# Performance work log

Hardware: AMD Instinct MI355X
Metric: run time of the kernel (lower is better)

The kernel has to match this reference:

```python
import jax, jax.numpy as jnp
import numpy as np


def setup_inputs() -> dict:
    key = jax.random.key(0)
    kq, kk, kv = jax.random.split(key, 3)
    B, T, H, D = 2, 4096, 8, 64
    q = jax.random.normal(kq, (B, T, H, D), dtype=jnp.float32)
    k = jax.random.normal(kk, (B, T, H, D), dtype=jnp.float32)
    v = jax.random.normal(kv, (B, T, H, D), dtype=jnp.float32)
    return {"q": q, "k": k, "v": v}


def reference(q, k, v):
    """Linear matrix-memory recurrence over the sequence:
       M_t = M_{t-1} + v_t k_t^T ;  y_t = M_t q_t
    q, k, v: [B, T, H, D] -> y: [B, T, H, D]
    """
    B, T, H, D = q.shape
    # time-major for scan: [T, B, H, D]
    qT = jnp.moveaxis(q, 1, 0)
    kT = jnp.moveaxis(k, 1, 0)
    vT = jnp.moveaxis(v, 1, 0)

    def step(M, qkv):
        q_t, k_t, v_t = qkv  # each [B, H, D]
        # update: M += v_t k_t^T  (outer product, 'bhd,bhe->bhde')
        M = M + v_t[..., :, None] * k_t[..., None, :]
        # apply: y_t = M q_t  ('bhde,bhe->bhd')
        y_t = jnp.einsum('bhde,bhe->bhd', M, q_t)
        return M, y_t

    M0 = jnp.zeros((B, H, D, D), dtype=q.dtype)
    _, ys = jax.lax.scan(step, M0, (qT, kT, vT))  # ys: [T, B, H, D]
    return jnp.moveaxis(ys, 0, 1)  # [B, T, H, D]
```

## Files before the change

kernel.cpp:

```cpp
#include <hip/hip_runtime.h>


#define B_   2
#define T_   4096
#define H_   8
#define D_   64
#define CH   64
#define NC   (T_ / CH)
#define BH   (B_ * H_)
#define SROW (H_ * D_)
#define SB   (T_ * H_ * D_)

typedef __attribute__((ext_vector_type(4))) float f32x4;
typedef __attribute__((ext_vector_type(8))) short bf16x8;

__device__ inline unsigned short f2bf(float f) {
  unsigned int u = __builtin_bit_cast(unsigned int, f);
  unsigned int r = (u + 0x7FFFu + ((u >> 16) & 1u)) >> 16;
  return (unsigned short)r;
}
__device__ inline float bf2f(unsigned short b) {
  unsigned int u = ((unsigned int)b) << 16;
  return __builtin_bit_cast(float, u);
}
__device__ inline void st4bf(unsigned short* p, float a, float b, float c, float d) {
  union { uint2 u; unsigned short s[4]; } x;
  x.s[0] = f2bf(a); x.s[1] = f2bf(b); x.s[2] = f2bf(c); x.s[3] = f2bf(d);
  *(uint2*)p = x.u;
}
__device__ inline bf16x8 ld128(const unsigned short* p) {
  union { uint4 u; bf16x8 v; } x;
  x.u = *(const uint4*)p;
  return x.v;
}
__device__ inline void unpackM(const uint4 a, const uint4 b, bf16x8& hi, bf16x8& lo) {
  unsigned xs[8] = { a.x, a.y, a.z, a.w, b.x, b.y, b.z, b.w };
  union { unsigned u[4]; bf16x8 v; } H, L;
#pragma unroll
  for (int i = 0; i < 4; ++i) {
    unsigned p0 = xs[2 * i], p1 = xs[2 * i + 1];
    H.u[i] = (p0 >> 16) | (p1 & 0xffff0000u);
    L.u[i] = (p0 & 0xffffu) | (p1 << 16);
  }
  hi = H.v; lo = L.v;
}


__global__ __launch_bounds__(256) void k_chunksum(const float* __restrict__ kp,
                                                  const float* __restrict__ vp,
                                                  unsigned short* __restrict__ Sp) {
  const int bid = blockIdx.x;
  const int c   = bid & 63;
  const int bh  = bid >> 6;
  const int b   = bh >> 3, h = bh & 7;
  const size_t base = (size_t)b * SB + (size_t)h * D_ + (size_t)(c * CH) * SROW;

  __shared__ __align__(16) unsigned short KT[4096], VT[4096];

  const int tid = threadIdx.x;
  const int l = tid & 63, w = tid >> 6;
  const int mlan = l & 15, qlan = l >> 4;

  {
    const int t0 = (tid >> 4) * 4;
    const int m0 = tid & 15;
    const int qs = (t0 >> 3) & 3, kbs = t0 >> 5, j0 = t0 & 4;
    float4 kr[4], vr[4];
#pragma unroll
    for (int i = 0; i < 4; ++i) {
      const size_t g = base + (size_t)(t0 + i) * SROW + 4 * m0;
      kr[i] = *(const float4*)(kp + g);
      vr[i] = *(const float4*)(vp + g);
    }
#pragma unroll
    for (int r = 0; r < 4; ++r) {
      const int d = 4 * m0 + r;
      const int slot = r * 16 + qs * 4 + (m0 & 3);
      const int addr = (((d >> 4) * 2 + kbs) * 64 + slot) * 8 + j0;
      st4bf(KT + addr, ((const float*)&kr[0])[r], ((const float*)&kr[1])[r],
                       ((const float*)&kr[2])[r], ((const float*)&kr[3])[r]);
      st4bf(VT + addr, ((const float*)&vr[0])[r], ((const float*)&vr[1])[r],
                       ((const float*)&vr[2])[r], ((const float*)&vr[3])[r]);
    }
  }
  __syncthreads();

  const int rslot = ((mlan & 3) << 4) + (qlan << 2) + (mlan >> 2);
  bf16x8 av[2];
  av[0] = ld128(VT + ((w * 2 + 0) * 64 + rslot) * 8);
  av[1] = ld128(VT + ((w * 2 + 1) * 64 + rslot) * 8);

  unsigned short* Sc = Sp + (size_t)bid * 4096;
#pragma unroll
  for (int te = 0; te < 4; ++te) {
    f32x4 acc = {0.f, 0.f, 0.f, 0.f};
#pragma unroll
    for (int kb = 0; kb < 2; ++kb) {
      bf16x8 bk = ld128(KT + ((te * 2 + kb) * 64 + rslot) * 8);
      acc = __builtin_amdgcn_mfma_f32_16x16x32_bf16(av[kb], bk, acc, 0, 0, 0);
    }
#pragma unroll
    for (int r = 0; r < 4; ++r)
      Sc[(16 * w + 4 * qlan + r) * 64 + 16 * te + mlan] = f2bf(acc[r]);
  }
}

__global__ __launch_bounds__(256) void k_prefix(const unsigned short* __restrict__ Sp,
                                                unsigned* __restrict__ Mp) {
  const int g = blockIdx.x * 256 + threadIdx.x;
  const int bh = g >> 12, e = g & 4095;
  const unsigned short* sp = Sp + (size_t)bh * (NC * 4096) + e;
  unsigned* mp = Mp + (size_t)bh * (NC * 4096) + e;
  float run = 0.f;
#pragma unroll
  for (int grp = 0; grp < 4; ++grp) {
    unsigned short sv[16];
#pragma unroll
    for (int i = 0; i < 16; ++i)
      sv[i] = sp[(size_t)(grp * 16 + i) * 4096];
#pragma unroll
    for (int i = 0; i < 16; ++i) {
      const unsigned short hi = f2bf(run);
      const unsigned short lo = f2bf(run - bf2f(hi));
      mp[(size_t)(grp * 16 + i) * 4096] = ((unsigned)hi << 16) | (unsigned)lo;
      run += bf2f(sv[i]);
    }
  }
}

__global__ __launch_bounds__(256) void k_output(const float* __restrict__ qp,
                                                const float* __restrict__ kp,
                                                const float* __restrict__ vp,
                                                const unsigned* __restrict__ Mp,
                                                float* __restrict__ yp) {
  const int bid = blockIdx.x;
  const int c   = bid & 63;
  const int bh  = bid >> 6;
  const int b   = bh >> 3, h = bh & 7;
  const size_t base = (size_t)b * SB + (size_t)h * D_ + (size_t)(c * CH) * SROW;

  __shared__ __align__(16) unsigned short QF[4096], KF[4096], VF[4096], PS[4096];

  const int tid = threadIdx.x;
  const int l = tid & 63, w = tid >> 6;
  const int mlan = l & 15, qlan = l >> 4;

  uint4 mA[8], mB[8];
#pragma unroll
  for (int td = 0; td < 4; ++td)
#pragma unroll
    for (int kb = 0; kb < 2; ++kb) {
      const uint4* mp = (const uint4*)(Mp + (size_t)bid * 4096
                                      + (16 * td + mlan) * 64 + 32 * kb + 8 * qlan);
      mA[td * 2 + kb] = mp[0];
      mB[td * 2 + kb] = mp[1];
    }

#pragma unroll
  for (int it = 0; it < 4; ++it) {
    const int f = tid + it * 256;
    const int t = f >> 4, m0 = f & 15;
    const int kb = m0 >> 3, qq = (m0 & 7) >> 1, j0 = (m0 & 1) * 4;
    const int addr = (((t >> 4) * 2 + kb) * 64 + ((t & 15) * 4 + qq)) * 8 + j0;
    const size_t g = base + (size_t)t * SROW + 4 * m0;
    float4 qv = *(const float4*)(qp + g);
    float4 kv = *(const float4*)(kp + g);
    st4bf(QF + addr, qv.x, qv.y, qv.z, qv.w);
    st4bf(KF + addr, kv.x, kv.y, kv.z, kv.w);
  }
  {
    const int s0 = (tid >> 4) * 4;
    const int m0 = tid & 15;
    const int qs = (s0 >> 3) & 3, kbs = s0 >> 5, j0 = s0 & 4;
    float4 vr[4];
#pragma unroll
    for (int i = 0; i < 4; ++i)
      vr[i] = *(const float4*)(vp + base + (size_t)(s0 + i) * SROW + 4 * m0);
#pragma unroll
    for (int r = 0; r < 4; ++r) {
      const int d = 4 * m0 + r;
      const int slot = r * 16 + qs * 4 + (m0 & 3);
      const int addr = (((d >> 4) * 2 + kbs) * 64 + slot) * 8 + j0;
      st4bf(VF + addr, ((const float*)&vr[0])[r], ((const float*)&vr[1])[r],
                       ((const float*)&vr[2])[r], ((const float*)&vr[3])[r]);
    }
  }
  __syncthreads();

  bf16x8 aq[2];
#pragma unroll
  for (int kb = 0; kb < 2; ++kb)
    aq[kb] = ld128(QF + ((w * 2 + kb) * 64 + (mlan * 4 + qlan)) * 8);

  f32x4 accP[4];
#pragma unroll
  for (int ts = 0; ts < 4; ++ts) accP[ts] = (f32x4){0.f, 0.f, 0.f, 0.f};
#pragma unroll
  for (int ts = 0; ts < 4; ++ts) {
    if (ts <= w) {
#pragma unroll
      for (int kb = 0; kb < 2; ++kb) {
        bf16x8 bk = ld128(KF + ((ts * 2 + kb) * 64 + (mlan * 4 + qlan)) * 8);
        accP[ts] = __builtin_amdgcn_mfma_f32_16x16x32_bf16(aq[kb], bk, accP[ts], 0, 0, 0);
      }
    }
  }
#pragma unroll
  for (int ts = 0; ts < 4; ++ts)
    if (ts == w) {
#pragma unroll
      for (int r = 0; r < 4; ++r)
        if (mlan > qlan * 4 + r) accP[ts][r] = 0.f;
    }

  {
    unsigned short* PSW = PS + w * 1024;
#pragma unroll
    for (int ts = 0; ts < 4; ++ts)
#pragma unroll
      for (int r = 0; r < 4; ++r)
        PSW[((2 * ts + (mlan >> 3)) * 16 + 4 * qlan + r) * 8 + (mlan & 7)] =
            f2bf(accP[ts][r]);
  }
  bf16x8 ap[2];
#pragma unroll
  for (int sb = 0; sb < 2; ++sb)
    ap[sb] = ld128(PS + w * 1024 + ((4 * sb + qlan) * 16 + mlan) * 8);

  const int rslot = ((mlan & 3) << 4) + (qlan << 2) + (mlan >> 2);

  f32x4 accY[4];
#pragma unroll
  for (int td = 0; td < 4; ++td) accY[td] = (f32x4){0.f, 0.f, 0.f, 0.f};

#pragma unroll
  for (int td = 0; td < 4; ++td)
#pragma unroll
    for (int sb = 0; sb < 2; ++sb) {
      bf16x8 bv = ld128(VF + ((td * 2 + sb) * 64 + rslot) * 8);
      accY[td] = __builtin_amdgcn_mfma_f32_16x16x32_bf16(ap[sb], bv, accY[td], 0, 0, 0);
    }
#pragma unroll
  for (int td = 0; td < 4; ++td)
#pragma unroll
    for (int kb = 0; kb < 2; ++kb) {
      bf16x8 bmh, bml;
      unpackM(mA[td * 2 + kb], mB[td * 2 + kb], bmh, bml);
      accY[td] = __builtin_amdgcn_mfma_f32_16x16x32_bf16(aq[kb], bmh, accY[td], 0, 0, 0);
      accY[td] = __builtin_amdgcn_mfma_f32_16x16x32_bf16(aq[kb], bml, accY[td], 0, 0, 0);
    }

#pragma unroll
  for (int td = 0; td < 4; ++td)
#pragma unroll
    for (int r = 0; r < 4; ++r)
      yp[base + (size_t)(16 * w + 4 * qlan + r) * SROW + 16 * td + mlan] = accY[td][r];
}

extern "C" void kernel_launch(void* const* d_in, const int* in_sizes, int n_in,
                              void* d_out, int out_size, void* d_ws, size_t ws_size,
                              hipStream_t stream) {
  const float* q = (const float*)d_in[0];
  const float* k = (const float*)d_in[1];
  const float* v = (const float*)d_in[2];
  float* y = (float*)d_out;
  unsigned short* S = (unsigned short*)d_ws;
  unsigned*       M = (unsigned*)((char*)d_ws + (32u << 20));

  k_chunksum<<<BH * NC, 256, 0, stream>>>(k, v, S);
  k_prefix  <<<256, 256, 0, stream>>>(S, M);
  k_output  <<<BH * NC, 256, 0, stream>>>(q, k, v, M, y);
}
```

Measured before the change: 111.4 us.

## Stage chunk-state M through LDS via async global_load_lds and load Q directly to registers

```diff
diff --git a/kernel.cpp b/kernel.cpp
--- a/kernel.cpp
+++ b/kernel.cpp
@@ -109,8 +109,9 @@
                                                 unsigned* __restrict__ Mp) {
   const int g = blockIdx.x * 256 + threadIdx.x;
   const int bh = g >> 12, e = g & 4095;
+  const int ep = e ^ (((e >> 6) & 7) << 2);
   const unsigned short* sp = Sp + (size_t)bh * (NC * 4096) + e;
-  unsigned* mp = Mp + (size_t)bh * (NC * 4096) + e;
+  unsigned* mp = Mp + (size_t)bh * (NC * 4096) + ep;
   float run = 0.f;
 #pragma unroll
   for (int grp = 0; grp < 4; ++grp) {
@@ -128,33 +129,32 @@
   }
 }
 
-__global__ __launch_bounds__(256) void k_output(const float* __restrict__ qp,
-                                                const float* __restrict__ kp,
-                                                const float* __restrict__ vp,
-                                                const unsigned* __restrict__ Mp,
-                                                float* __restrict__ yp) {
+__global__ __launch_bounds__(256, 4) void k_output(const float* __restrict__ qp,
+                                                   const float* __restrict__ kp,
+                                                   const float* __restrict__ vp,
+                                                   const unsigned* __restrict__ Mp,
+                                                   float* __restrict__ yp) {
   const int bid = blockIdx.x;
   const int c   = bid & 63;
   const int bh  = bid >> 6;
   const int b   = bh >> 3, h = bh & 7;
   const size_t base = (size_t)b * SB + (size_t)h * D_ + (size_t)(c * CH) * SROW;
 
-  __shared__ __align__(16) unsigned short QF[4096], KF[4096], VF[4096], PS[4096];
+  __shared__ __align__(16) unsigned short KF[4096], VF[4096], PS[4096];
+  __shared__ __align__(16) unsigned MF[4096];
 
   const int tid = threadIdx.x;
   const int l = tid & 63, w = tid >> 6;
   const int mlan = l & 15, qlan = l >> 4;
 
-  uint4 mA[8], mB[8];
-#pragma unroll
-  for (int td = 0; td < 4; ++td)
-#pragma unroll
-    for (int kb = 0; kb < 2; ++kb) {
-      const uint4* mp = (const uint4*)(Mp + (size_t)bid * 4096
-                                      + (16 * td + mlan) * 64 + 32 * kb + 8 * qlan);
-      mA[td * 2 + kb] = mp[0];
-      mB[td * 2 + kb] = mp[1];
-    }
+#pragma unroll
+  for (int i = 0; i < 4; ++i) {
+    const unsigned* g = Mp + (size_t)bid * 4096 + (w * 4 + i) * 256 + l * 4;
+    __builtin_amdgcn_global_load_lds(
+        (const __attribute__((address_space(1))) unsigned*)g,
+        (__attribute__((address_space(3))) unsigned*)(MF + (w * 4 + i) * 256),
+        16, 0, 0);
+  }
 
 #pragma unroll
   for (int it = 0; it < 4; ++it) {
@@ -162,10 +162,8 @@
     const int t = f >> 4, m0 = f & 15;
     const int kb = m0 >> 3, qq = (m0 & 7) >> 1, j0 = (m0 & 1) * 4;
     const int addr = (((t >> 4) * 2 + kb) * 64 + ((t & 15) * 4 + qq)) * 8 + j0;
-    const size_t g = base + (size_t)t * SROW + 4 * m0;
-    float4 qv = *(const float4*)(qp + g);
-    float4 kv = *(const float4*)(kp + g);
-    st4bf(QF + addr, qv.x, qv.y, qv.z, qv.w);
+    const size_t gaddr = base + (size_t)t * SROW + 4 * m0;
+    float4 kv = *(const float4*)(kp + gaddr);
     st4bf(KF + addr, kv.x, kv.y, kv.z, kv.w);
   }
   {
@@ -185,12 +183,21 @@
                        ((const float*)&vr[2])[r], ((const float*)&vr[3])[r]);
     }
   }
+
+  bf16x8 aq[2];
+  {
+    const float* qrow = qp + base + (size_t)(16 * w + mlan) * SROW + 8 * qlan;
+#pragma unroll
+    for (int kb = 0; kb < 2; ++kb) {
+      float4 a0 = *(const float4*)(qrow + 32 * kb);
+      float4 a1 = *(const float4*)(qrow + 32 * kb + 4);
+      union { unsigned short s[8]; bf16x8 v; } P;
+      P.s[0] = f2bf(a0.x); P.s[1] = f2bf(a0.y); P.s[2] = f2bf(a0.z); P.s[3] = f2bf(a0.w);
+      P.s[4] = f2bf(a1.x); P.s[5] = f2bf(a1.y); P.s[6] = f2bf(a1.z); P.s[7] = f2bf(a1.w);
+      aq[kb] = P.v;
+    }
+  }
   __syncthreads();
-
-  bf16x8 aq[2];
-#pragma unroll
-  for (int kb = 0; kb < 2; ++kb)
-    aq[kb] = ld128(QF + ((w * 2 + kb) * 64 + (mlan * 4 + qlan)) * 8);
 
   f32x4 accP[4];
 #pragma unroll
@@ -240,12 +247,17 @@
       bf16x8 bv = ld128(VF + ((td * 2 + sb) * 64 + rslot) * 8);
       accY[td] = __builtin_amdgcn_mfma_f32_16x16x32_bf16(ap[sb], bv, accY[td], 0, 0, 0);
     }
+
+  const int m7 = mlan & 7;
 #pragma unroll
   for (int td = 0; td < 4; ++td)
 #pragma unroll
     for (int kb = 0; kb < 2; ++kb) {
+      const int mb = (16 * td + mlan) * 64 + kb * 32 + ((qlan ^ (m7 >> 1)) << 3);
+      const uint4 va = *(const uint4*)(MF + mb + ((m7 & 1) << 2));
+      const uint4 vb = *(const uint4*)(MF + mb + (((m7 & 1) ^ 1) << 2));
       bf16x8 bmh, bml;
-      unpackM(mA[td * 2 + kb], mB[td * 2 + kb], bmh, bml);
+      unpackM(va, vb, bmh, bml);
       accY[td] = __builtin_amdgcn_mfma_f32_16x16x32_bf16(aq[kb], bmh, accY[td], 0, 0, 0);
       accY[td] = __builtin_amdgcn_mfma_f32_16x16x32_bf16(aq[kb], bml, accY[td], 0, 0, 0);
     }
```

New measurement: 109.9 us. About the same (-1.3%).
